# Kernel tuning notes

Hardware: AMD Instinct MI355X
Metric: run time of the kernel (lower is better)

Reference implementation:

```python
import jax, jax.numpy as jnp
import numpy as np

TAU = 0.2
VTH = 0.3


def setup_inputs() -> dict:
    key = jax.random.key(0)
    x = jax.random.normal(key, (32, 128, 32, 32, 8), dtype=jnp.float32)
    return {"x": x}


def reference(x):
    # x: [B, C, H, W, T]; LIF membrane update scanned over time (last axis).
    xt = jnp.moveaxis(x, -1, 0)  # [T, B, C, H, W]
    u0 = jnp.zeros(x.shape[:-1], dtype=x.dtype)
    o0 = jnp.zeros(x.shape[:-1], dtype=x.dtype)

    def step(carry, x_t):
        u_prev, o_prev = carry
        u = TAU * u_prev * (1.0 - o_prev) + x_t
        o = (u - VTH > 0).astype(x_t.dtype)  # hard threshold spike
        return (u, o), o

    _, out_t = jax.lax.scan(step, (u0, o0), xt)
    return jnp.moveaxis(out_t, 0, -1)  # [B, C, H, W, T]
```

## Files before the change

kernel.cpp:

```cpp
#include <hip/hip_runtime.h>

#define TAU 0.2f
#define VTH 0.3f

#define PPB 256
#define PADF 12

typedef float v4f __attribute__((ext_vector_type(4)));

__global__ __launch_bounds__(256) void LIFSpike_73864847556979_kernel(
    const float* __restrict__ x, float* __restrict__ out) {
    __shared__ float lds[PPB * PADF];
    const int t = threadIdx.x;
    const size_t base_f4 = (size_t)blockIdx.x * (PPB * 2);

    const v4f* __restrict__ xin = (const v4f*)x + base_f4;
    v4f* __restrict__ xout = (v4f*)out + base_f4;

    v4f a = xin[t];
    v4f b = xin[t + 256];
    const int j0 = t, j1 = t + 256;
    *(v4f*)&lds[(j0 >> 1) * PADF + (j0 & 1) * 4] = a;
    *(v4f*)&lds[(j1 >> 1) * PADF + (j1 & 1) * 4] = b;
    __syncthreads();

    v4f lo = *(const v4f*)&lds[t * PADF];
    v4f hi = *(const v4f*)&lds[t * PADF + 4];
    float v[8] = {lo.x, lo.y, lo.z, lo.w, hi.x, hi.y, hi.z, hi.w};
    float r[8];
    float u = 0.0f, o = 0.0f;
#pragma unroll
    for (int k = 0; k < 8; ++k) {
        u = TAU * u * (1.0f - o) + v[k];
        o = (u > VTH) ? 1.0f : 0.0f;
        r[k] = o;
    }
    *(v4f*)&lds[t * PADF] = (v4f){r[0], r[1], r[2], r[3]};
    *(v4f*)&lds[t * PADF + 4] = (v4f){r[4], r[5], r[6], r[7]};
    __syncthreads();

    v4f c = *(const v4f*)&lds[(j0 >> 1) * PADF + (j0 & 1) * 4];
    v4f d = *(const v4f*)&lds[(j1 >> 1) * PADF + (j1 & 1) * 4];
    __builtin_nontemporal_store(c, &xout[t]);
    __builtin_nontemporal_store(d, &xout[t + 256]);
}

extern "C" void kernel_launch(void* const* d_in, const int* in_sizes, int n_in,
                              void* d_out, int out_size, void* d_ws, size_t ws_size,
                              hipStream_t stream) {
    const float* x = (const float*)d_in[0];
    float* out = (float*)d_out;
    int n_pixels = in_sizes[0] / 8;
    int grid = n_pixels / PPB;
    LIFSpike_73864847556979_kernel<<<grid, PPB, 0, stream>>>(x, out);
}
```

Baseline: 227.9 us.

## Replace LDS transpose with grid-stride loop and register prefetch

Removes the shared-memory transpose: each thread now loads whole pixels (8 contiguous floats each) straight from global memory. A fixed grid of 1024 blocks loops 4 times, loading the next chunk into registers while the current one is processed. This avoids LDS traffic and barriers, but lanes now access strided 128-byte chunks, which hurts coalescing. The grid size is hardcoded for this input shape.

```diff
diff --git a/kernel.cpp b/kernel.cpp
--- a/kernel.cpp
+++ b/kernel.cpp
@@ -3,46 +3,55 @@
 #define TAU 0.2f
 #define VTH 0.3f
 
-#define PPB 256
-#define PADF 12
+typedef float v4f __attribute__((ext_vector_type(4)));
 
-typedef float v4f __attribute__((ext_vector_type(4)));
+#define BLOCKS 1024
+#define THREADS 256
+#define PX_PER_ITER 4
+#define ITERS 4
 
 __global__ __launch_bounds__(256) void LIFSpike_73864847556979_kernel(
     const float* __restrict__ x, float* __restrict__ out) {
-    __shared__ float lds[PPB * PADF];
-    const int t = threadIdx.x;
-    const size_t base_f4 = (size_t)blockIdx.x * (PPB * 2);
+    const int tid = blockIdx.x * THREADS + threadIdx.x;
+    const size_t nthreads = (size_t)BLOCKS * THREADS;
 
-    const v4f* __restrict__ xin = (const v4f*)x + base_f4;
-    v4f* __restrict__ xout = (v4f*)out + base_f4;
+    const v4f* __restrict__ xin = (const v4f*)x;
+    v4f* __restrict__ xout = (v4f*)out;
 
-    v4f a = xin[t];
-    v4f b = xin[t + 256];
-    const int j0 = t, j1 = t + 256;
-    *(v4f*)&lds[(j0 >> 1) * PADF + (j0 & 1) * 4] = a;
-    *(v4f*)&lds[(j1 >> 1) * PADF + (j1 & 1) * 4] = b;
-    __syncthreads();
+    v4f cur[8], nxt[8];
+    size_t base = (size_t)tid * 8;
 
-    v4f lo = *(const v4f*)&lds[t * PADF];
-    v4f hi = *(const v4f*)&lds[t * PADF + 4];
-    float v[8] = {lo.x, lo.y, lo.z, lo.w, hi.x, hi.y, hi.z, hi.w};
-    float r[8];
-    float u = 0.0f, o = 0.0f;
 #pragma unroll
-    for (int k = 0; k < 8; ++k) {
-        u = TAU * u * (1.0f - o) + v[k];
-        o = (u > VTH) ? 1.0f : 0.0f;
-        r[k] = o;
+    for (int j = 0; j < 8; ++j) cur[j] = xin[base + j];
+
+#pragma unroll 1
+    for (int it = 0; it < ITERS; ++it) {
+        const size_t nbase = base + nthreads * 8;
+        if (it + 1 < ITERS) {
+#pragma unroll
+            for (int j = 0; j < 8; ++j) nxt[j] = xin[nbase + j];
+        }
+#pragma unroll
+        for (int p = 0; p < PX_PER_ITER; ++p) {
+            v4f lo = cur[p * 2], hi = cur[p * 2 + 1];
+            float v[8] = {lo.x, lo.y, lo.z, lo.w, hi.x, hi.y, hi.z, hi.w};
+            float r[8];
+            float u = 0.0f, o = 0.0f;
+#pragma unroll
+            for (int k = 0; k < 8; ++k) {
+                u = TAU * u * (1.0f - o) + v[k];
+                o = (u > VTH) ? 1.0f : 0.0f;
+                r[k] = o;
+            }
+            v4f ro = {r[0], r[1], r[2], r[3]};
+            v4f rh = {r[4], r[5], r[6], r[7]};
+            __builtin_nontemporal_store(ro, &xout[base + p * 2]);
+            __builtin_nontemporal_store(rh, &xout[base + p * 2 + 1]);
+        }
+#pragma unroll
+        for (int j = 0; j < 8; ++j) cur[j] = nxt[j];
+        base = nbase;
     }
-    *(v4f*)&lds[t * PADF] = (v4f){r[0], r[1], r[2], r[3]};
-    *(v4f*)&lds[t * PADF + 4] = (v4f){r[4], r[5], r[6], r[7]};
-    __syncthreads();
-
-    v4f c = *(const v4f*)&lds[(j0 >> 1) * PADF + (j0 & 1) * 4];
-    v4f d = *(const v4f*)&lds[(j1 >> 1) * PADF + (j1 & 1) * 4];
-    __builtin_nontemporal_store(c, &xout[t]);
-    __builtin_nontemporal_store(d, &xout[t + 256]);
 }
 
 extern "C" void kernel_launch(void* const* d_in, const int* in_sizes, int n_in,
@@ -50,7 +59,5 @@
                               hipStream_t stream) {
     const float* x = (const float*)d_in[0];
     float* out = (float*)d_out;
-    int n_pixels = in_sizes[0] / 8;
-    int grid = n_pixels / PPB;
-    LIFSpike_73864847556979_kernel<<<grid, PPB, 0, stream>>>(x, out);
+    LIFSpike_73864847556979_kernel<<<BLOCKS, THREADS, 0, stream>>>(x, out);
 }
```

After: 520.2 us. 2.28x slower.
